# Performance work log

Measured on AMD Instinct MI355X. Metric: run time of the kernel, lower is better.

Reference implementation:

```python
import jax, jax.numpy as jnp
import numpy as np

A = 9            # cfg.anchors.num
K = 1000         # cfg.frcnn.nms.output_size
IOU_THR = 0.7    # cfg.frcnn.nms.iou
NEG = jnp.float32(-1e30)


def setup_inputs() -> dict:
    key = jax.random.key(0)
    ks = jax.random.split(key, 8)
    B, H, W, C = 1, 100, 152, 1024
    feat = jax.random.normal(ks[0], (B, H, W, C), jnp.float32)
    # conv kernels with small (0.01) std, matching typical RPN truncated-normal init
    w_cls = jax.random.normal(ks[1], (C, 2 * A), jnp.float32) * 0.01
    b_cls = jnp.zeros((2 * A,), jnp.float32)
    w_bbox = jax.random.normal(ks[2], (C, 4 * A), jnp.float32) * 0.01
    b_bbox = jnp.zeros((4 * A,), jnp.float32)
    img_sz = jnp.array([800.0, 1216.0], jnp.float32)
    N = B * H * W * A  # 136800 anchors, [x0, y0, x1, y1]
    cx = jax.random.uniform(ks[3], (N,), jnp.float32, 0.0, 800.0)
    cy = jax.random.uniform(ks[4], (N,), jnp.float32, 0.0, 1216.0)
    sh = jax.random.uniform(ks[5], (N,), jnp.float32, 16.0, 128.0)
    sw = jax.random.uniform(ks[6], (N,), jnp.float32, 16.0, 128.0)
    anchors = jnp.stack([cx - 0.5 * sh, cy - 0.5 * sw, cx + 0.5 * sh, cy + 0.5 * sw], axis=1)
    return {"rpn_feature": feat, "anchors": anchors, "img_sz": img_sz,
            "w_cls": w_cls, "b_cls": b_cls, "w_bbox": w_bbox, "b_bbox": b_bbox}


def convert_and_clip(anchors, pred, img_sz):
    # anchors [N,4]; decode deltas (tx pairs with h, ty with w, per original code)
    w = anchors[:, 3] - anchors[:, 1] + 1.0
    h = anchors[:, 2] - anchors[:, 0] + 1.0
    x = anchors[:, 0] + 0.5 * h
    y = anchors[:, 1] + 0.5 * w
    tx, ty, tw, th = pred[:, 0], pred[:, 1], pred[:, 2], pred[:, 3]
    x_pred = tx * h + x
    y_pred = ty * w + y
    w_pred = jnp.exp(tw) * w
    h_pred = jnp.exp(th) * h
    x0 = jnp.maximum(x_pred - 0.5 * h_pred, 0.0)
    x1 = jnp.minimum(x_pred + 0.5 * h_pred, img_sz[0])
    y0 = jnp.maximum(y_pred - 0.5 * w_pred, 0.0)
    y1 = jnp.minimum(y_pred + 0.5 * w_pred, img_sz[1])
    return jnp.stack([x0, y0, x1, y1], axis=1)


def greedy_nms(boxes, scores, k, iou_thr):
    # boxes [N,4] = [c0, c1, c2, c3]; IoU is symmetric in coord convention
    x0, y0, x1, y1 = boxes[:, 0], boxes[:, 1], boxes[:, 2], boxes[:, 3]
    areas = (x1 - x0) * (y1 - y0)

    def step(s, _):
        i = jnp.argmax(s)
        valid = s[i] > NEG * 0.5
        iw = jnp.maximum(jnp.minimum(x1, x1[i]) - jnp.maximum(x0, x0[i]), 0.0)
        ih = jnp.maximum(jnp.minimum(y1, y1[i]) - jnp.maximum(y0, y0[i]), 0.0)
        inter = iw * ih
        iou = inter / (areas + areas[i] - inter + 1e-9)
        s = jnp.where((iou >= iou_thr) & valid, NEG, s)
        s = s.at[i].set(NEG)
        return s, (i, valid)

    _, (idx, valid) = jax.lax.scan(step, scores, None, length=k)
    return idx, valid


def reference(rpn_feature, anchors, img_sz, w_cls, b_cls, w_bbox, b_bbox):
    # 1x1 convs == per-pixel GEMM
    cls_score = jnp.einsum('bhwc,co->bhwo', rpn_feature, w_cls) + b_cls       # [B,H,W,2A]
    cls_prob2 = jax.nn.softmax(cls_score.reshape(-1, 2), axis=-1)             # pairwise softmax
    cls_pred = jnp.argmax(cls_prob2, axis=-1)
    cls_prob = cls_prob2.reshape(cls_score.shape)
    bbox_pred = (jnp.einsum('bhwc,co->bhwo', rpn_feature, w_bbox) + b_bbox).reshape(-1, 4)
    fg = cls_prob[:, :, :, A:].reshape(-1)                                    # foreground scores
    boxes = convert_and_clip(anchors, bbox_pred, img_sz)                      # [N,4]
    idx, valid = greedy_nms(boxes, fg, K, IOU_THR)
    proposals = jnp.where(valid[:, None], boxes[idx], 0.0)                    # [K,4]
    return proposals, idx, cls_prob, cls_pred, bbox_pred
```

## Files before the change

### kernel.cpp

```cpp
#include <hip/hip_runtime.h>
#include <cstdint>
#include <cstddef>

#define NPOS   15200
#define NANCH  136800
#define KDIM   1024
#define NCLS   18
#define NBB    36
#define KS     8
#define KCH    (KDIM / KS)
#define KSTEP  32
#define MTILE  256
#define MCAP   4096
#define NROW   2048
#define NWRD   32
#define TARGET_SEL 3072
#define KSEL   1000
#define HBINS  8192

typedef unsigned long long u64;

#define OFF_PROP    0
#define OFF_IDX     4000
#define OFF_CLSPROB 5000
#define OFF_CLSPRED 278600
#define OFF_BB      415400

struct Ctrl {
  int selCount;
  int bstar;
  int pad[14];
};

__device__ inline unsigned int fkey(float f) {
  unsigned int b = __float_as_uint(f);
  return (b & 0x80000000u) ? ~b : (b | 0x80000000u);
}

__global__ __launch_bounds__(256) void gemm6(const float* __restrict__ feat,
                                             const float* __restrict__ wcls,
                                             const float* __restrict__ wbb,
                                             double* __restrict__ diffPart,
                                             float* __restrict__ clsPart,
                                             float* __restrict__ bbPart) {
  __shared__ __align__(16) float  fS[KSTEP * MTILE];
  __shared__ __align__(16) float  wL[KCH * 72];
  __shared__ __align__(16) double wDL[KCH * 10];
  const int t = threadIdx.x;
  const int lane = t & 63;
  const int wv   = t >> 6;
  const int P0 = blockIdx.x * MTILE;
  const int k0 = blockIdx.y * KCH;

  for (int idx = t; idx < KCH * NCLS; idx += 256) {
    int k = idx / NCLS, c = idx % NCLS;
    wL[k * 72 + c] = wcls[(size_t)(k0 + k) * NCLS + c];
  }
  for (int idx = t; idx < KCH * NBB; idx += 256) {
    int k = idx / NBB, c = idx % NBB;
    wL[k * 72 + ((c < 18) ? (24 + c) : (48 + (c - 18)))] = wbb[(size_t)(k0 + k) * NBB + c];
  }
  for (int idx = t; idx < KCH * 9; idx += 256) {
    int k = idx / 9, j = idx % 9;
    int cC = 9 + j, cD = cC ^ 1;
    wDL[k * 10 + j] = (double)wcls[(size_t)(k0 + k) * NCLS + cC] -
                      (double)wcls[(size_t)(k0 + k) * NCLS + cD];
  }

  double accd[4][9];
  float  accf[4][18];
#pragma unroll
  for (int p = 0; p < 4; ++p) {
#pragma unroll
    for (int j = 0; j < 9; ++j) accd[p][j] = 0.0;
#pragma unroll
    for (int c = 0; c < 18; ++c) accf[p][c] = 0.f;
  }

  float4 fr[8];
  auto LOADF = [&](int kb) {
#pragma unroll
    for (int j = 0; j < 8; ++j) {
      int idx = j * 256 + t;
      int p = idx >> 3, q = idx & 7;
      int gp = P0 + p;
      fr[j] = make_float4(0.f, 0.f, 0.f, 0.f);
      if (gp < NPOS) fr[j] = *(const float4*)(feat + (size_t)gp * KDIM + kb + q * 4);
    }
  };
  auto WRITEF = [&]() {
#pragma unroll
    for (int j = 0; j < 8; ++j) {
      int idx = j * 256 + t;
      int p = idx >> 3, q = idx & 7;
      const float vv[4] = {fr[j].x, fr[j].y, fr[j].z, fr[j].w};
#pragma unroll
      for (int i = 0; i < 4; ++i) {
        int kk = q * 4 + i;
        int swz = ((kk >> 2) & 7) << 2;
        fS[kk * MTILE + (p ^ swz)] = vv[i];
      }
    }
  };

  LOADF(k0);
  const int NSTEP = KCH / KSTEP;
  for (int s = 0; s < NSTEP; ++s) {
    __syncthreads();
    WRITEF();
    if (s + 1 < NSTEP) LOADF(k0 + (s + 1) * KSTEP);
    __syncthreads();

    const int kb = s * KSTEP;
    if (wv == 0) {
#pragma unroll 2
      for (int kk = 0; kk < KSTEP; ++kk) {
        int swz = ((kk >> 2) & 7) << 2;
        const float4 f4 = *(const float4*)&fS[kk * MTILE + ((lane * 4) ^ swz)];
        const double f[4] = {(double)f4.x, (double)f4.y, (double)f4.z, (double)f4.w};
        const double* wd = &wDL[(kb + kk) * 10];
        const double2 w01 = *(const double2*)&wd[0];
        const double2 w23 = *(const double2*)&wd[2];
        const double2 w45 = *(const double2*)&wd[4];
        const double2 w67 = *(const double2*)&wd[6];
        const double  w8  = wd[8];
        const double w[9] = {w01.x, w01.y, w23.x, w23.y, w45.x, w45.y, w67.x, w67.y, w8};
#pragma unroll
        for (int p = 0; p < 4; ++p)
#pragma unroll
          for (int j = 0; j < 9; ++j) accd[p][j] += f[p] * w[j];
      }
    } else {
      const int cb = (wv == 1) ? 0 : ((wv == 2) ? 24 : 48);
#pragma unroll 2
      for (int kk = 0; kk < KSTEP; ++kk) {
        int swz = ((kk >> 2) & 7) << 2;
        const float4 f4 = *(const float4*)&fS[kk * MTILE + ((lane * 4) ^ swz)];
        const float f[4] = {f4.x, f4.y, f4.z, f4.w};
        const float* wp = &wL[(kb + kk) * 72 + cb];
        const float4 w0 = *(const float4*)&wp[0];
        const float4 w1 = *(const float4*)&wp[4];
        const float4 w2 = *(const float4*)&wp[8];
        const float4 w3 = *(const float4*)&wp[12];
        const float2 w4 = *(const float2*)&wp[16];
        const float w[18] = {w0.x, w0.y, w0.z, w0.w, w1.x, w1.y, w1.z, w1.w,
                             w2.x, w2.y, w2.z, w2.w, w3.x, w3.y, w3.z, w3.w,
                             w4.x, w4.y};
#pragma unroll
        for (int p = 0; p < 4; ++p)
#pragma unroll
          for (int c = 0; c < 18; ++c) accf[p][c] += f[p] * w[c];
      }
    }
  }

#pragma unroll
  for (int i = 0; i < 4; ++i) {
    int gp = P0 + lane * 4 + i;
    if (gp >= NPOS) continue;
    if (wv == 0) {
      double* o = diffPart + ((size_t)blockIdx.y * NPOS + gp) * 9;
#pragma unroll
      for (int j = 0; j < 9; ++j) o[j] = accd[i][j];
    } else if (wv == 1) {
      float* o = clsPart + ((size_t)blockIdx.y * NPOS + gp) * NCLS;
#pragma unroll
      for (int c = 0; c < 18; ++c) o[c] = accf[i][c];
    } else {
      float* o = bbPart + ((size_t)blockIdx.y * NPOS + gp) * NBB + (wv - 2) * 18;
#pragma unroll
      for (int c = 0; c < 18; ++c) o[c] = accf[i][c];
    }
  }
}

__global__ __launch_bounds__(256) void epilogue(const double* __restrict__ diffPart, const float* __restrict__ clsPart,
                         const float* __restrict__ bbPart,
                         const float* __restrict__ bcls, const float* __restrict__ bbb,
                         const float* __restrict__ anchors, const float* __restrict__ imgsz,
                         float* __restrict__ out, double* __restrict__ dkeys,
                         float* __restrict__ bx0, float* __restrict__ by0,
                         float* __restrict__ bx1, float* __restrict__ by1,
                         float* __restrict__ bar, int* __restrict__ hist) {
  __shared__ int hS[HBINS];
  const int t = threadIdx.x;
  for (int i = t; i < HBINS; i += 256) hS[i] = 0;
  __syncthreads();

  int n = blockIdx.x * 256 + t;
  if (n < NANCH) {
    int pos = n / 9, j = n % 9;
    int cA = 2 * j, cB = 2 * j + 1, cC = 9 + j, cD = cC ^ 1;
    float sA = bcls[cA], sB = bcls[cB];
#pragma unroll
    for (int ks = 0; ks < KS; ++ks) {
      const float* pp = clsPart + ((size_t)ks * NPOS + pos) * NCLS;
      sA += pp[cA]; sB += pp[cB];
    }
    double d = (double)bcls[cC] - (double)bcls[cD];
#pragma unroll
    for (int ks = 0; ks < KS; ++ks)
      d += diffPart[((size_t)ks * NPOS + pos) * 9 + j];

    out[OFF_CLSPROB + (size_t)pos * 18 + cA] = 1.0f / (1.0f + expf(sB - sA));
    out[OFF_CLSPROB + (size_t)pos * 18 + cB] = 1.0f / (1.0f + expf(sA - sB));
    out[OFF_CLSPRED + n] = (sB > sA) ? 1.0f : 0.0f;
    dkeys[n] = d;
    atomicAdd(&hS[fkey((float)d) >> 19], 1);

    float tb[4];
#pragma unroll
    for (int m = 0; m < 4; ++m) {
      float s = bbb[4 * j + m];
#pragma unroll
      for (int ks = 0; ks < KS; ++ks)
        s += bbPart[((size_t)ks * NPOS + pos) * NBB + 4 * j + m];
      tb[m] = s;
      out[OFF_BB + (size_t)n * 4 + m] = s;
    }
    float4 a = *(const float4*)(anchors + (size_t)n * 4);
    float w = a.w - a.y + 1.0f;
    float h = a.z - a.x + 1.0f;
    float x = a.x + 0.5f * h;
    float y = a.y + 0.5f * w;
    float xp = tb[0] * h + x;
    float yp = tb[1] * w + y;
    float wp = expf(tb[2]) * w;
    float hp = expf(tb[3]) * h;
    float X0 = fmaxf(xp - 0.5f * hp, 0.f);
    float X1 = fminf(xp + 0.5f * hp, imgsz[0]);
    float Y0 = fmaxf(yp - 0.5f * wp, 0.f);
    float Y1 = fminf(yp + 0.5f * wp, imgsz[1]);
    bx0[n] = X0; by0[n] = Y0; bx1[n] = X1; by1[n] = Y1;
    bar[n] = (X1 - X0) * (Y1 - Y0);
  }

  __syncthreads();
  for (int i = t; i < HBINS; i += 256) {
    int v = hS[i];
    if (v) atomicAdd(&hist[i], v);
  }
}

__global__ void scank(const int* __restrict__ hist, Ctrl* __restrict__ ctrl) {
  __shared__ int hS[HBINS];
  __shared__ int cS[256];
  int t = threadIdx.x;
  for (int i = t; i < HBINS; i += 256) hS[i] = hist[i];
  __syncthreads();
  int s = 0;
  for (int b = 0; b < 32; ++b) s += hS[t * 32 + b];
  cS[t] = s;
  __syncthreads();
  if (t == 0) {
    int acc = 0;
    for (int cb = 255; cb >= 0; --cb) {
      int cs = cS[cb];
      if (acc + cs >= TARGET_SEL || acc + cs > MCAP) {
        int bstar = cb * 32;
        for (int b = cb * 32 + 31; b >= cb * 32; --b) {
          int h = hS[b];
          if (acc + h > MCAP) { bstar = b + 1; break; }
          acc += h;
          if (acc >= TARGET_SEL) { bstar = b; break; }
        }
        ctrl->bstar = bstar;
        return;
      }
      acc += cs;
    }
    ctrl->bstar = 0;
  }
}

__global__ __launch_bounds__(256) void compactk(const double* __restrict__ dkeys, Ctrl* __restrict__ ctrl,
                                                int* __restrict__ sel) {
  __shared__ int wofs[4];
  __shared__ int base;
  const int t = threadIdx.x;
  const int lane = t & 63, wv = t >> 6;
  int n = blockIdx.x * 256 + t;
  bool pick = false;
  if (n < NANCH) {
    unsigned int u = fkey((float)dkeys[n]);
    pick = ((int)(u >> 19) >= ctrl->bstar);
  }
  u64 b = __ballot(pick);
  int wpre = __popcll(b & ((lane == 0) ? 0ull : (~0ull >> (64 - lane))));
  if (lane == 0) wofs[wv] = __popcll(b);
  __syncthreads();
  if (t == 0) {
    int c0 = wofs[0], c1 = wofs[1], c2 = wofs[2], c3 = wofs[3];
    int tot = c0 + c1 + c2 + c3;
    wofs[0] = 0; wofs[1] = c0; wofs[2] = c0 + c1; wofs[3] = c0 + c1 + c2;
    base = tot ? atomicAdd(&ctrl->selCount, tot) : 0;
  }
  __syncthreads();
  if (pick) {
    int slot = base + wofs[wv] + wpre;
    if (slot < MCAP) sel[slot] = n;
  }
}

__global__ __launch_bounds__(256) void rankk(const double* __restrict__ dkeys,
                                             const int* __restrict__ sel,
                                             const Ctrl* __restrict__ ctrl,
                                             int* __restrict__ rank) {
  int C = ctrl->selCount; if (C > MCAP) C = MCAP;
  if ((int)(blockIdx.x << 8) >= C || (int)(blockIdx.y << 8) >= C) return;
  __shared__ double kS[256];
  __shared__ int    iS[256];
  const int t = threadIdx.x;
  int j = blockIdx.y * 256 + t;
  if (j < C) { int n = sel[j]; kS[t] = dkeys[n]; iS[t] = n; }
  else       { kS[t] = -1.0e300; iS[t] = NANCH + j; }
  int i = blockIdx.x * 256 + t;
  double ki; int ii;
  if (i < C) { int n = sel[i]; ki = dkeys[n]; ii = n; }
  else       { ki = -1.0e300; ii = NANCH + i; }
  __syncthreads();
  int cnt = 0;
#pragma unroll 8
  for (int q = 0; q < 256; ++q) {
    double kq = kS[q]; int iq = iS[q];
    cnt += (int)((kq > ki) || (kq == ki && iq < ii));
  }
  atomicAdd(&rank[i], cnt);
}

__global__ __launch_bounds__(256) void scatterk(const int* __restrict__ sel,
                                                const Ctrl* __restrict__ ctrl,
                                                const int* __restrict__ rank,
                                                int* __restrict__ sidx,
                                                float* __restrict__ sx0, float* __restrict__ sy0,
                                                float* __restrict__ sx1, float* __restrict__ sy1,
                                                float* __restrict__ sar,
                                                const float* __restrict__ bx0, const float* __restrict__ by0,
                                                const float* __restrict__ bx1, const float* __restrict__ by1,
                                                const float* __restrict__ bar) {
  int i = blockIdx.x * 256 + threadIdx.x;
  if (i >= MCAP) return;
  int C = ctrl->selCount;
  if (C > MCAP) C = MCAP;
  if (i < C) {
    int r = rank[i];
    if (r < 0 || r >= MCAP) return;
    int n = sel[i];
    sidx[r] = n;
    sx0[r] = bx0[n]; sy0[r] = by0[n]; sx1[r] = bx1[n]; sy1[r] = by1[n]; sar[r] = bar[n];
  } else {
    sidx[i] = 0x7FFFFFFF;
    sx0[i] = 0.f; sy0[i] = 0.f; sx1[i] = 0.f; sy1[i] = 0.f; sar[i] = 0.f;
  }
}

__global__ __launch_bounds__(256) void iouk2(const float* __restrict__ sx0, const float* __restrict__ sy0,
                                             const float* __restrict__ sx1, const float* __restrict__ sy1,
                                             const float* __restrict__ sar,
                                             u64* __restrict__ mask) {
  __shared__ float X0[NROW], Y0[NROW], X1[NROW], Y1[NROW], AR[NROW];
  int t = threadIdx.x;
  for (int i = t; i < NROW; i += 256) {
    X0[i] = sx0[i]; Y0[i] = sy0[i]; X1[i] = sx1[i]; Y1[i] = sy1[i]; AR[i] = sar[i];
  }
  __syncthreads();
  int r0 = blockIdx.x * 16;
  for (int task = t; task < 16 * NWRD; task += 256) {
    int r = r0 + (task >> 5);
    int w = task & 31;
    float x0r = X0[r], y0r = Y0[r], x1r = X1[r], y1r = Y1[r], arr = AR[r];
    u64 bits = 0ull;
#pragma unroll 16
    for (int jj = 0; jj < 64; ++jj) {
      int jc = (w << 6) + jj;
      float iw = fminf(x1r, X1[jc]) - fmaxf(x0r, X0[jc]);
      iw = fmaxf(iw, 0.f);
      float ih = fminf(y1r, Y1[jc]) - fmaxf(y0r, Y0[jc]);
      ih = fmaxf(ih, 0.f);
      float inter = iw * ih;
      float iou = inter / (AR[jc] + arr - inter + 1e-9f);
      bits |= ((u64)(iou >= 0.7f)) << jj;
    }
    mask[(size_t)r * NWRD + w] = bits;
  }
}

__global__ __launch_bounds__(64) void nmsk2(const u64* __restrict__ mask,
                                            const int* __restrict__ sidx,
                                            const float* __restrict__ sx0, const float* __restrict__ sy0,
                                            const float* __restrict__ sx1, const float* __restrict__ sy1,
                                            const float* __restrict__ sar,
                                            const Ctrl* __restrict__ ctrl,
                                            float* __restrict__ out) {
  __shared__ int keptPos[KSEL];
  const int lane = threadIdx.x;
  const int h = lane >> 5, m = lane & 31;
  int C = ctrl->selCount; if (C > MCAP) C = MCAP;
  int kept = 0;
  u64 sup = 0;
  const int nwin = min((C + 63) >> 6, NROW >> 6);

  u64 bufA[32], bufB[32], dgA = 0, dgB = 0;

  auto ISSUE = [&](u64* buf, u64& dg, int w) {
    const u64* base = mask + ((size_t)(w * 64 + h * 32) * NWRD + m);
#pragma unroll
    for (int j = 0; j < 32; ++j) buf[j] = base[(size_t)j * NWRD];
    dg = mask[((size_t)(w * 64 + lane)) * NWRD + w];
  };

  auto PROCW = [&](u64* buf, u64 dg, int w) {
    u64 swin = __shfl(sup, w);
    int rem = C - w * 64;
    u64 vmask = (rem >= 64) ? ~0ull : ((1ull << rem) - 1);
    u64 cand = (~swin) & vmask;
    u64 keep = 0;
    if (cand) {
      u64 gt = (lane == 63) ? 0ull : (~0ull << (lane + 1));
      bool own = (cand >> lane) & 1;
      u64 bad = __ballot(own && ((dg & cand & gt) != 0ull));
      if (bad == 0ull) {
        keep = cand;
      } else {
        u64 cur = cand;
        for (int j = 0; j < 64; ++j) {
          if ((cur >> j) & 1) {
            keep |= 1ull << j;
            u64 dj = __shfl(dg, j);
            u64 gtj = (j == 63) ? 0ull : (~0ull << (j + 1));
            cur &= ~(dj & gtj);
          }
        }
      }
    }
    int pc = __popcll(keep);
    int need = KSEL - kept;
    while (pc > need) { keep &= ~(1ull << (63 - __clzll(keep))); --pc; }
    if ((keep >> lane) & 1) {
      int p = kept + __popcll(keep & ((1ull << lane) - 1ull));
      keptPos[p] = w * 64 + lane;
    }
    u64 orv = 0;
    u64 kmh = h ? (keep >> 32) : (keep & 0xffffffffull);
#pragma unroll
    for (int j = 0; j < 32; ++j)
      if ((kmh >> j) & 1) orv |= buf[j];
    orv |= __shfl_xor(orv, 32);
    sup |= orv;
    kept += pc;
  };

  if (nwin > 0) {
    ISSUE(bufA, dgA, 0);
    int w = 0;
    while (w < nwin && kept < KSEL) {
      if (w + 1 < nwin) ISSUE(bufB, dgB, w + 1);
      PROCW(bufA, dgA, w); ++w;
      if (w >= nwin || kept >= KSEL) break;
      if (w + 1 < nwin) ISSUE(bufA, dgA, w + 1);
      PROCW(bufB, dgB, w); ++w;
    }
  }

  for (int r = NROW; r < C && kept < KSEL; ++r) {
    float x0 = sx0[r], y0 = sy0[r], x1 = sx1[r], y1 = sy1[r], ar = sar[r];
    bool supr = false;
    for (int b = lane; b < kept; b += 64) {
      int kp = keptPos[b];
      float iw = fminf(x1, sx1[kp]) - fmaxf(x0, sx0[kp]);
      iw = fmaxf(iw, 0.f);
      float ih = fminf(y1, sy1[kp]) - fmaxf(y0, sy0[kp]);
      ih = fmaxf(ih, 0.f);
      float inter = iw * ih;
      float iou = inter / (sar[kp] + ar - inter + 1e-9f);
      if (iou >= 0.7f) supr = true;
    }
    if (__ballot(supr) != 0ull) continue;
    if (lane == 0) keptPos[kept] = r;
    ++kept;
  }

  __syncthreads();
  for (int q = lane; q < KSEL; q += 64) {
    if (q < kept) {
      int kp = keptPos[q];
      int n = sidx[kp];
      out[OFF_PROP + 4 * q + 0] = sx0[kp];
      out[OFF_PROP + 4 * q + 1] = sy0[kp];
      out[OFF_PROP + 4 * q + 2] = sx1[kp];
      out[OFF_PROP + 4 * q + 3] = sy1[kp];
      out[OFF_IDX + q] = (float)n;
    } else {
      out[OFF_PROP + 4 * q + 0] = 0.f;
      out[OFF_PROP + 4 * q + 1] = 0.f;
      out[OFF_PROP + 4 * q + 2] = 0.f;
      out[OFF_PROP + 4 * q + 3] = 0.f;
      out[OFF_IDX + q] = 0.f;
    }
  }
}

__global__ void badws(float* out) {
  if (threadIdx.x == 0 && blockIdx.x == 0) out[0] = 1.0e8f;
}

extern "C" void kernel_launch(void* const* d_in, const int* in_sizes, int n_in,
                              void* d_out, int out_size, void* d_ws, size_t ws_size,
                              hipStream_t stream) {
  (void)in_sizes; (void)n_in; (void)out_size;
  const float* feat    = (const float*)d_in[0];
  const float* anchors = (const float*)d_in[1];
  const float* imgsz   = (const float*)d_in[2];
  const float* wcls    = (const float*)d_in[3];
  const float* bcls    = (const float*)d_in[4];
  const float* wbb     = (const float*)d_in[5];
  const float* bbb     = (const float*)d_in[6];
  float* out = (float*)d_out;
  char* ws = (char*)d_ws;

  const size_t o_diff   = 0;
  const size_t o_cls    = o_diff + (size_t)KS * NPOS * 9 * 8;
  const size_t o_bb     = o_cls + (size_t)KS * NPOS * NCLS * 4;
  const size_t o_dkeys  = o_bb + (size_t)KS * NPOS * NBB * 4;
  const size_t o_bx0    = o_dkeys + (size_t)NANCH * 8;
  const size_t o_by0    = o_bx0 + (size_t)NANCH * 4;
  const size_t o_bx1    = o_by0 + (size_t)NANCH * 4;
  const size_t o_by1    = o_bx1 + (size_t)NANCH * 4;
  const size_t o_bar    = o_by1 + (size_t)NANCH * 4;
  const size_t o_hist   = o_bar + (size_t)NANCH * 4;
  const size_t o_ctrl   = o_hist + (size_t)HBINS * 4;
  const size_t o_rank   = o_ctrl + 256;
  const size_t o_sel    = o_rank + (size_t)MCAP * 4;
  const size_t o_sidx   = o_sel + (size_t)MCAP * 4;
  const size_t o_sx0    = o_sidx + (size_t)MCAP * 4;
  const size_t o_sy0    = o_sx0 + (size_t)MCAP * 4;
  const size_t o_sx1    = o_sy0 + (size_t)MCAP * 4;
  const size_t o_sy1    = o_sx1 + (size_t)MCAP * 4;
  const size_t o_sar    = o_sy1 + (size_t)MCAP * 4;
  const size_t o_mask   = o_sar + (size_t)MCAP * 4;
  const size_t need     = o_mask + (size_t)NROW * NWRD * 8;

  if (ws_size < need) {
    badws<<<dim3(1), dim3(64), 0, stream>>>(out);
    return;
  }

  double* diffPart = (double*)(ws + o_diff);
  float*  clsPart  = (float*)(ws + o_cls);
  float*  bbPart   = (float*)(ws + o_bb);
  double* dkeys    = (double*)(ws + o_dkeys);
  float*  bx0      = (float*)(ws + o_bx0);
  float*  by0      = (float*)(ws + o_by0);
  float*  bx1      = (float*)(ws + o_bx1);
  float*  by1      = (float*)(ws + o_by1);
  float*  bar      = (float*)(ws + o_bar);
  int*    hist     = (int*)(ws + o_hist);
  Ctrl*   ctrl     = (Ctrl*)(ws + o_ctrl);
  int*    rank     = (int*)(ws + o_rank);
  int*    sel      = (int*)(ws + o_sel);
  int*    sidx     = (int*)(ws + o_sidx);
  float*  sx0      = (float*)(ws + o_sx0);
  float*  sy0      = (float*)(ws + o_sy0);
  float*  sx1      = (float*)(ws + o_sx1);
  float*  sy1      = (float*)(ws + o_sy1);
  float*  sar      = (float*)(ws + o_sar);
  u64*    mask     = (u64*)(ws + o_mask);

  hipMemsetAsync(ws + o_hist, 0, (size_t)HBINS * 4 + 256 + (size_t)MCAP * 4, stream);

  gemm6<<<dim3((NPOS + MTILE - 1) / MTILE, KS), dim3(256), 0, stream>>>(
      feat, wcls, wbb, diffPart, clsPart, bbPart);
  epilogue<<<dim3((NANCH + 255) / 256), dim3(256), 0, stream>>>(
      diffPart, clsPart, bbPart, bcls, bbb, anchors, imgsz, out, dkeys, bx0, by0, bx1, by1, bar, hist);
  scank<<<dim3(1), dim3(256), 0, stream>>>(hist, ctrl);
  compactk<<<dim3((NANCH + 255) / 256), dim3(256), 0, stream>>>(dkeys, ctrl, sel);
  rankk<<<dim3(MCAP / 256, MCAP / 256), dim3(256), 0, stream>>>(dkeys, sel, ctrl, rank);
  scatterk<<<dim3(MCAP / 256), dim3(256), 0, stream>>>(sel, ctrl, rank, sidx,
                                                       sx0, sy0, sx1, sy1, sar,
                                                       bx0, by0, bx1, by1, bar);
  iouk2<<<dim3(NROW / 16), dim3(256), 0, stream>>>(sx0, sy0, sx1, sy1, sar, mask);
  nmsk2<<<dim3(1), dim3(64), 0, stream>>>(mask, sidx, sx0, sy0, sx1, sy1, sar, ctrl, out);
}
```

Before: 170.0 us.

## Fold memset, scan and scatter into neighbouring kernels via last-block tickets

Replaces the host memset by zeroing the histogram/control/rank region inside the first GEMM block. The histogram scan moves into the epilogue and the scatter into the rank kernel, each run by the last block to finish as detected by an atomic ticket counter. This cuts the kernel-launch count and the gaps between launches, at the cost of threadfences, atomics, and a single block doing the serial tail work.

```diff
diff --git a/kernel.cpp b/kernel.cpp
--- a/kernel.cpp
+++ b/kernel.cpp
@@ -17,6 +17,7 @@
 #define TARGET_SEL 3072
 #define KSEL   1000
 #define HBINS  8192
+#define ZWORDS ((HBINS * 4 + 256 + MCAP * 4) / 4)
 
 typedef unsigned long long u64;
 
@@ -29,7 +30,9 @@
 struct Ctrl {
   int selCount;
   int bstar;
-  int pad[14];
+  int ticket1;
+  int ticket2;
+  int pad[12];
 };
 
 __device__ inline unsigned int fkey(float f) {
@@ -42,7 +45,8 @@
                                              const float* __restrict__ wbb,
                                              double* __restrict__ diffPart,
                                              float* __restrict__ clsPart,
-                                             float* __restrict__ bbPart) {
+                                             float* __restrict__ bbPart,
+                                             int* __restrict__ zbase) {
   __shared__ __align__(16) float  fS[KSTEP * MTILE];
   __shared__ __align__(16) float  wL[KCH * 72];
   __shared__ __align__(16) double wDL[KCH * 10];
@@ -51,6 +55,10 @@
   const int wv   = t >> 6;
   const int P0 = blockIdx.x * MTILE;
   const int k0 = blockIdx.y * KCH;
+
+  if (blockIdx.x == 0 && blockIdx.y == 0) {
+    for (int i = t; i < ZWORDS; i += 256) zbase[i] = 0;
+  }
 
   for (int idx = t; idx < KCH * NCLS; idx += 256) {
     int k = idx / NCLS, c = idx % NCLS;
@@ -181,8 +189,11 @@
                          float* __restrict__ out, double* __restrict__ dkeys,
                          float* __restrict__ bx0, float* __restrict__ by0,
                          float* __restrict__ bx1, float* __restrict__ by1,
-                         float* __restrict__ bar, int* __restrict__ hist) {
+                         float* __restrict__ bar, int* __restrict__ hist,
+                         Ctrl* __restrict__ ctrl) {
   __shared__ int hS[HBINS];
+  __shared__ int cS[256];
+  __shared__ int lastFlag;
   const int t = threadIdx.x;
   for (int i = t; i < HBINS; i += 256) hS[i] = 0;
   __syncthreads();
@@ -240,13 +251,14 @@
     int v = hS[i];
     if (v) atomicAdd(&hist[i], v);
   }
-}
-
-__global__ void scank(const int* __restrict__ hist, Ctrl* __restrict__ ctrl) {
-  __shared__ int hS[HBINS];
-  __shared__ int cS[256];
-  int t = threadIdx.x;
-  for (int i = t; i < HBINS; i += 256) hS[i] = hist[i];
+
+  __threadfence();
+  __syncthreads();
+  if (t == 0) lastFlag = (atomicAdd(&ctrl->ticket1, 1) == (int)gridDim.x - 1);
+  __syncthreads();
+  if (!lastFlag) return;
+  __threadfence();
+  for (int i = t; i < HBINS; i += 256) hS[i] = atomicAdd(&hist[i], 0);
   __syncthreads();
   int s = 0;
   for (int b = 0; b < 32; ++b) s += hS[t * 32 + b];
@@ -254,10 +266,11 @@
   __syncthreads();
   if (t == 0) {
     int acc = 0;
+    int bstar = 0;
     for (int cb = 255; cb >= 0; --cb) {
       int cs = cS[cb];
       if (acc + cs >= TARGET_SEL || acc + cs > MCAP) {
-        int bstar = cb * 32;
+        bstar = cb * 32;
         for (int b = cb * 32 + 31; b >= cb * 32; --b) {
           int h = hS[b];
           if (acc + h > MCAP) { bstar = b + 1; break; }
@@ -302,55 +315,58 @@
   }
 }
 
-__global__ __launch_bounds__(256) void rankk(const double* __restrict__ dkeys,
-                                             const int* __restrict__ sel,
-                                             const Ctrl* __restrict__ ctrl,
-                                             int* __restrict__ rank) {
-  int C = ctrl->selCount; if (C > MCAP) C = MCAP;
-  if ((int)(blockIdx.x << 8) >= C || (int)(blockIdx.y << 8) >= C) return;
+__global__ __launch_bounds__(256) void rankscatterk(const double* __restrict__ dkeys,
+                                                    const int* __restrict__ sel,
+                                                    Ctrl* __restrict__ ctrl,
+                                                    int* __restrict__ rank,
+                                                    int* __restrict__ sidx,
+                                                    float* __restrict__ sx0, float* __restrict__ sy0,
+                                                    float* __restrict__ sx1, float* __restrict__ sy1,
+                                                    float* __restrict__ sar,
+                                                    const float* __restrict__ bx0, const float* __restrict__ by0,
+                                                    const float* __restrict__ bx1, const float* __restrict__ by1,
+                                                    const float* __restrict__ bar) {
   __shared__ double kS[256];
   __shared__ int    iS[256];
+  __shared__ int lastFlag;
   const int t = threadIdx.x;
-  int j = blockIdx.y * 256 + t;
-  if (j < C) { int n = sel[j]; kS[t] = dkeys[n]; iS[t] = n; }
-  else       { kS[t] = -1.0e300; iS[t] = NANCH + j; }
-  int i = blockIdx.x * 256 + t;
-  double ki; int ii;
-  if (i < C) { int n = sel[i]; ki = dkeys[n]; ii = n; }
-  else       { ki = -1.0e300; ii = NANCH + i; }
-  __syncthreads();
-  int cnt = 0;
+  int C = ctrl->selCount; if (C > MCAP) C = MCAP;
+
+  if ((int)(blockIdx.x << 8) < C && (int)(blockIdx.y << 8) < C) {
+    int j = blockIdx.y * 256 + t;
+    if (j < C) { int n = sel[j]; kS[t] = dkeys[n]; iS[t] = n; }
+    else       { kS[t] = -1.0e300; iS[t] = NANCH + j; }
+    int i = blockIdx.x * 256 + t;
+    double ki; int ii;
+    if (i < C) { int n = sel[i]; ki = dkeys[n]; ii = n; }
+    else       { ki = -1.0e300; ii = NANCH + i; }
+    __syncthreads();
+    int cnt = 0;
 #pragma unroll 8
-  for (int q = 0; q < 256; ++q) {
-    double kq = kS[q]; int iq = iS[q];
-    cnt += (int)((kq > ki) || (kq == ki && iq < ii));
-  }
-  atomicAdd(&rank[i], cnt);
-}
-
-__global__ __launch_bounds__(256) void scatterk(const int* __restrict__ sel,
-                                                const Ctrl* __restrict__ ctrl,
-                                                const int* __restrict__ rank,
-                                                int* __restrict__ sidx,
-                                                float* __restrict__ sx0, float* __restrict__ sy0,
-                                                float* __restrict__ sx1, float* __restrict__ sy1,
-                                                float* __restrict__ sar,
-                                                const float* __restrict__ bx0, const float* __restrict__ by0,
-                                                const float* __restrict__ bx1, const float* __restrict__ by1,
-                                                const float* __restrict__ bar) {
-  int i = blockIdx.x * 256 + threadIdx.x;
-  if (i >= MCAP) return;
-  int C = ctrl->selCount;
-  if (C > MCAP) C = MCAP;
-  if (i < C) {
-    int r = rank[i];
-    if (r < 0 || r >= MCAP) return;
-    int n = sel[i];
-    sidx[r] = n;
-    sx0[r] = bx0[n]; sy0[r] = by0[n]; sx1[r] = bx1[n]; sy1[r] = by1[n]; sar[r] = bar[n];
-  } else {
-    sidx[i] = 0x7FFFFFFF;
-    sx0[i] = 0.f; sy0[i] = 0.f; sx1[i] = 0.f; sy1[i] = 0.f; sar[i] = 0.f;
+    for (int q = 0; q < 256; ++q) {
+      double kq = kS[q]; int iq = iS[q];
+      cnt += (int)((kq > ki) || (kq == ki && iq < ii));
+    }
+    atomicAdd(&rank[i], cnt);
+  }
+
+  __threadfence();
+  __syncthreads();
+  if (t == 0) lastFlag = (atomicAdd(&ctrl->ticket2, 1) == (int)(gridDim.x * gridDim.y) - 1);
+  __syncthreads();
+  if (!lastFlag) return;
+  __threadfence();
+  for (int i = t; i < MCAP; i += 256) {
+    if (i < C) {
+      int r = atomicAdd(&rank[i], 0);
+      if (r < 0 || r >= MCAP) continue;
+      int n = sel[i];
+      sidx[r] = n;
+      sx0[r] = bx0[n]; sy0[r] = by0[n]; sx1[r] = bx1[n]; sy1[r] = by1[n]; sar[r] = bar[n];
+    } else {
+      sidx[i] = 0x7FFFFFFF;
+      sx0[i] = 0.f; sy0[i] = 0.f; sx1[i] = 0.f; sy1[i] = 0.f; sar[i] = 0.f;
+    }
   }
 }
 
@@ -566,18 +582,14 @@
   float*  sar      = (float*)(ws + o_sar);
   u64*    mask     = (u64*)(ws + o_mask);
 
-  hipMemsetAsync(ws + o_hist, 0, (size_t)HBINS * 4 + 256 + (size_t)MCAP * 4, stream);
-
   gemm6<<<dim3((NPOS + MTILE - 1) / MTILE, KS), dim3(256), 0, stream>>>(
-      feat, wcls, wbb, diffPart, clsPart, bbPart);
+      feat, wcls, wbb, diffPart, clsPart, bbPart, (int*)(ws + o_hist));
   epilogue<<<dim3((NANCH + 255) / 256), dim3(256), 0, stream>>>(
-      diffPart, clsPart, bbPart, bcls, bbb, anchors, imgsz, out, dkeys, bx0, by0, bx1, by1, bar, hist);
-  scank<<<dim3(1), dim3(256), 0, stream>>>(hist, ctrl);
+      diffPart, clsPart, bbPart, bcls, bbb, anchors, imgsz, out, dkeys,
+      bx0, by0, bx1, by1, bar, hist, ctrl);
   compactk<<<dim3((NANCH + 255) / 256), dim3(256), 0, stream>>>(dkeys, ctrl, sel);
-  rankk<<<dim3(MCAP / 256, MCAP / 256), dim3(256), 0, stream>>>(dkeys, sel, ctrl, rank);
-  scatterk<<<dim3(MCAP / 256), dim3(256), 0, stream>>>(sel, ctrl, rank, sidx,
-                                                       sx0, sy0, sx1, sy1, sar,
-                                                       bx0, by0, bx1, by1, bar);
+  rankscatterk<<<dim3(MCAP / 256, MCAP / 256), dim3(256), 0, stream>>>(
+      dkeys, sel, ctrl, rank, sidx, sx0, sy0, sx1, sy1, sar, bx0, by0, bx1, by1, bar);
   iouk2<<<dim3(NROW / 16), dim3(256), 0, stream>>>(sx0, sy0, sx1, sy1, sar, mask);
   nmsk2<<<dim3(1), dim3(64), 0, stream>>>(mask, sidx, sx0, sy0, sx1, sy1, sar, ctrl, out);
 }
```

Result: slower. 244.0 us (+43.5%).
